# Kernel optimization log

Measured on AMD Instinct MI355X. Metric: run time of the kernel, lower is better.

Reference implementation:

```python
import jax, jax.numpy as jnp
import numpy as np

# Hyperparameters matching GyroLoss(__init__)
W = 1.0e6        # w
MIN_N = 4        # min_N -> min_train_freq = 16
MAX_N = 5        # max_N -> max_train_freq = 32
DT = 0.01        # dt (100 Hz IMU)
HUBER = 0.005    # huber delta
N0 = 5           # warm-up steps dropped from the residual
MIN_TRAIN_FREQ = 2 ** MIN_N


def _skew(v):
    # v: [M,3] -> [M,3,3] skew-symmetric matrices
    x, y, z = v[..., 0], v[..., 1], v[..., 2]
    o = jnp.zeros_like(x)
    return jnp.stack([
        jnp.stack([o, -z,  y], -1),
        jnp.stack([z,  o, -x], -1),
        jnp.stack([-y, x,  o], -1),
    ], -2)


def so3_exp(phi):
    # Rodrigues formula, phi: [M,3] -> R: [M,3,3]
    sq = jnp.sum(phi * phi, -1, keepdims=True)          # [M,1]
    angle = jnp.sqrt(jnp.maximum(sq, 1e-16))
    small = sq < 1e-12
    a = jnp.where(small, 1.0, angle)
    s = jnp.where(small, 1.0 - sq / 6.0, jnp.sin(a) / a)
    c = jnp.where(small, 0.5 - sq / 24.0, (1.0 - jnp.cos(a)) / (a * a))
    K = _skew(phi)
    I = jnp.eye(3, dtype=phi.dtype)
    return I + s[..., None] * K + c[..., None] * jnp.matmul(K, K)


def so3_log(R):
    # R: [M,3,3] -> phi: [M,3]
    tr = R[..., 0, 0] + R[..., 1, 1] + R[..., 2, 2]
    cos = jnp.clip(0.5 * (tr - 1.0), -1.0 + 1e-7, 1.0 - 1e-7)
    angle = jnp.arccos(cos)
    s = angle / (2.0 * jnp.sin(angle))
    vee = jnp.stack([
        R[..., 2, 1] - R[..., 1, 2],
        R[..., 0, 2] - R[..., 2, 0],
        R[..., 1, 0] - R[..., 0, 1],
    ], -1)
    return s[..., None] * vee


def _bmtm(a, b):
    # batched a^T @ b for [M,3,3]
    return jnp.einsum('nij,nik->njk', a, b)


def _f_huber(rs):
    # SmoothL1Loss (beta=1, mean reduction) on rs/HUBER vs zeros, scaled by w*huber^2
    z = rs / HUBER
    az = jnp.abs(z)
    l = jnp.mean(jnp.where(az < 1.0, 0.5 * z * z, az - 0.5))
    return W * l * HUBER ** 2


def setup_inputs() -> dict:
    key = jax.random.key(0)
    k1, k2, k3 = jax.random.split(key, 3)
    N, T = 64, 32768  # T divisible by 2**MAX_N
    xs = jax.random.normal(k1, (N, T, 3), dtype=jnp.float32)
    dp = jax.random.normal(k2, (1, 3), dtype=jnp.float32)  # unused by forward
    hat_xs = jax.random.normal(k3, (N, T, 3), dtype=jnp.float32)
    return {"xs": xs, "dp": dp, "hat_xs": hat_xs}


def reference(xs, dp, hat_xs):
    N = xs.shape[0]
    # ground-truth increments at min_train_freq stride -> rotations
    xs_r = so3_exp(xs[:, ::MIN_TRAIN_FREQ].reshape(-1, 3))       # [N*T/16,3,3]
    # predicted gyro -> per-step rotation increments
    Om = so3_exp((DT * hat_xs).reshape(-1, 3))                    # [N*T,3,3]
    # tree reduction: compose adjacent rotations min_N times
    for _ in range(MIN_N):
        Om = jnp.matmul(Om[::2], Om[1::2])
    rs = so3_log(_bmtm(Om, xs_r)).reshape(N, -1, 3)[:, N0:]
    loss = _f_huber(rs)
    for k in range(MIN_N, MAX_N):
        Om = jnp.matmul(Om[::2], Om[1::2])
        xs_r = jnp.matmul(xs_r[::2], xs_r[1::2])
        rs = so3_log(_bmtm(Om, xs_r)).reshape(N, -1, 3)[:, N0:]
        loss = loss + _f_huber(rs) / 2.0 ** (k - MIN_N + 1)
    return loss
```

## Files before the change

### kernel.cpp

```cpp
#include <hip/hip_runtime.h>
#include <math.h>

#define NSEQ 64
#define TLEN 32768
#define G16_PER_SEQ 2048
#define NG16 (NSEQ * G16_PER_SEQ)
#define N0 5
#define DT 0.01f
#define HUBER_INV 200.0f

__device__ __constant__ float C16 = 25.0f / (64.0f * 2043.0f * 3.0f);
__device__ __constant__ float C32 = 12.5f / (64.0f * 1019.0f * 3.0f);

__device__ __forceinline__ void mat_mul3(const float* A, const float* B, float* C) {
#pragma unroll
    for (int i = 0; i < 3; ++i) {
#pragma unroll
        for (int j = 0; j < 3; ++j) {
            C[3 * i + j] = A[3 * i + 0] * B[0 + j]
                         + A[3 * i + 1] * B[3 + j]
                         + A[3 * i + 2] * B[6 + j];
        }
    }
}

__device__ __forceinline__ void so3_exp_dev(float x, float y, float z, float* R) {
    float sq = x * x + y * y + z * z;
    float angle = sqrtf(fmaxf(sq, 1e-16f));
    bool small = sq < 1e-12f;
    float a = small ? 1.0f : angle;
    float sn, cs;
    __sincosf(a, &sn, &cs);
    float s = small ? (1.0f - sq * (1.0f / 6.0f)) : (sn / a);
    float c = small ? (0.5f - sq * (1.0f / 24.0f)) : ((1.0f - cs) / (a * a));
    float cxx = c * x * x, cyy = c * y * y, czz = c * z * z;
    float cxy = c * x * y, cxz = c * x * z, cyz = c * y * z;
    float sx = s * x, sy = s * y, sz = s * z;
    R[0] = 1.0f - cyy - czz; R[1] = cxy - sz;          R[2] = cxz + sy;
    R[3] = cxy + sz;         R[4] = 1.0f - cxx - czz;  R[5] = cyz - sx;
    R[6] = cxz - sy;         R[7] = cyz + sx;          R[8] = 1.0f - cxx - cyy;
}

__device__ __forceinline__ float huber3_bmtm_log(const float* Om, const float* Xr) {
    float M[9];
#pragma unroll
    for (int j = 0; j < 3; ++j) {
#pragma unroll
        for (int k = 0; k < 3; ++k) {
            M[3 * j + k] = Om[0 + j] * Xr[0 + k]
                         + Om[3 + j] * Xr[3 + k]
                         + Om[6 + j] * Xr[6 + k];
        }
    }
    float tr = M[0] + M[4] + M[8];
    float cosv = 0.5f * (tr - 1.0f);
    cosv = fminf(fmaxf(cosv, -1.0f + 1e-7f), 1.0f - 1e-7f);
    float angle = acosf(cosv);
    float sn = sqrtf(fmaxf(1.0f - cosv * cosv, 0.0f));
    float sfac = angle / (2.0f * sn);
    float v[3];
    v[0] = sfac * (M[7] - M[5]);
    v[1] = sfac * (M[2] - M[6]);
    v[2] = sfac * (M[3] - M[1]);
    float acc = 0.0f;
#pragma unroll
    for (int t = 0; t < 3; ++t) {
        float zz = v[t] * HUBER_INV;
        float az = fabsf(zz);
        acc += (az < 1.0f) ? 0.5f * zz * zz : az - 0.5f;
    }
    return acc;
}

__global__ void zero_out_kernel(float* out, int n) {
    int i = blockIdx.x * blockDim.x + threadIdx.x;
    if (i < n) out[i] = 0.0f;
}

__global__ __launch_bounds__(256) void gyro_loss_kernel(const float* __restrict__ xs,
                                                        const float* __restrict__ hat_xs,
                                                        float* __restrict__ out) {
    const int g = blockIdx.x * blockDim.x + threadIdx.x;

    const float4* hp = reinterpret_cast<const float4*>(hat_xs) + (size_t)g * 12;
    float hbuf[48];
#pragma unroll
    for (int q = 0; q < 12; ++q) {
        float4 vv = hp[q];
        hbuf[4 * q + 0] = vv.x; hbuf[4 * q + 1] = vv.y;
        hbuf[4 * q + 2] = vv.z; hbuf[4 * q + 3] = vv.w;
    }

    float Om[9];
    so3_exp_dev(DT * hbuf[0], DT * hbuf[1], DT * hbuf[2], Om);
#pragma unroll
    for (int i = 1; i < 16; ++i) {
        float Ri[9], tmp[9];
        so3_exp_dev(DT * hbuf[3 * i + 0], DT * hbuf[3 * i + 1], DT * hbuf[3 * i + 2], Ri);
        mat_mul3(Om, Ri, tmp);
#pragma unroll
        for (int t = 0; t < 9; ++t) Om[t] = tmp[t];
    }

    float4 xv = *(reinterpret_cast<const float4*>(xs) + (size_t)g * 12);
    float Xr[9];
    so3_exp_dev(xv.x, xv.y, xv.z, Xr);

    float partial = 0.0f;
    const int j = g & (G16_PER_SEQ - 1);
    if (j >= N0) partial += C16 * huber3_bmtm_log(Om, Xr);

    float OmN[9], XrN[9];
#pragma unroll
    for (int t = 0; t < 9; ++t) {
        OmN[t] = __shfl_down(Om[t], 1);
        XrN[t] = __shfl_down(Xr[t], 1);
    }
    if ((g & 1) == 0) {
        float Om32[9], Xr32[9];
        mat_mul3(Om, OmN, Om32);
        mat_mul3(Xr, XrN, Xr32);
        const int j2 = (g >> 1) & ((G16_PER_SEQ / 2) - 1);
        if (j2 >= N0) partial += C32 * huber3_bmtm_log(Om32, Xr32);
    }

#pragma unroll
    for (int off = 32; off > 0; off >>= 1) partial += __shfl_down(partial, off);

    __shared__ float wsum[4];
    const int lane = threadIdx.x & 63;
    const int wid = threadIdx.x >> 6;
    if (lane == 0) wsum[wid] = partial;
    __syncthreads();
    if (threadIdx.x == 0) {
        atomicAdd(out, wsum[0] + wsum[1] + wsum[2] + wsum[3]);
    }
}

extern "C" void kernel_launch(void* const* d_in, const int* in_sizes, int n_in,
                              void* d_out, int out_size, void* d_ws, size_t ws_size,
                              hipStream_t stream) {
    const float* xs     = (const float*)d_in[0];
    const float* hat_xs = (const float*)d_in[2];
    float* out = (float*)d_out;

    zero_out_kernel<<<1, 64, 0, stream>>>(out, out_size);
    gyro_loss_kernel<<<NG16 / 256, 256, 0, stream>>>(xs, hat_xs, out);
}
```

Baseline: 95.54 us.

## Split 16-step rotation chain across 4 lanes with shuffle tree and LDS staging

Each 16-step group is now handled by four threads that each compose four rotations, then combine them in order through xor-shuffle matrix products. The 32-step level reuses the same shuffle combine instead of a shift-down pair. hat_xs is staged through LDS with coalesced float4 loads. The global atomic is replaced by per-block partials summed in a second kernel. This gives four times more threads with shorter dependency chains and fewer registers per thread, at the cost of redundant xs loads and exp work on idle lanes plus an extra launch.

```diff
diff --git a/kernel.cpp b/kernel.cpp
--- a/kernel.cpp
+++ b/kernel.cpp
@@ -5,6 +5,10 @@
 #define TLEN 32768
 #define G16_PER_SEQ 2048
 #define NG16 (NSEQ * G16_PER_SEQ)
+#define STEPS_PER_THREAD 4
+#define NTHREADS (NG16 * 4)
+#define BLOCK 256
+#define NBLOCKS (NTHREADS / BLOCK)
 #define N0 5
 #define DT 0.01f
 #define HUBER_INV 200.0f
@@ -58,83 +62,95 @@
     float angle = acosf(cosv);
     float sn = sqrtf(fmaxf(1.0f - cosv * cosv, 0.0f));
     float sfac = angle / (2.0f * sn);
-    float v[3];
-    v[0] = sfac * (M[7] - M[5]);
-    v[1] = sfac * (M[2] - M[6]);
-    v[2] = sfac * (M[3] - M[1]);
+    float v0 = sfac * (M[7] - M[5]);
+    float v1 = sfac * (M[2] - M[6]);
+    float v2 = sfac * (M[3] - M[1]);
     float acc = 0.0f;
 #pragma unroll
     for (int t = 0; t < 3; ++t) {
-        float zz = v[t] * HUBER_INV;
+        float zz = (t == 0 ? v0 : (t == 1 ? v1 : v2)) * HUBER_INV;
         float az = fabsf(zz);
         acc += (az < 1.0f) ? 0.5f * zz * zz : az - 0.5f;
     }
     return acc;
 }
 
-__global__ void zero_out_kernel(float* out, int n) {
-    int i = blockIdx.x * blockDim.x + threadIdx.x;
-    if (i < n) out[i] = 0.0f;
+__device__ __forceinline__ void ordered_combine(float* A, int mask, bool upper) {
+    float L[9], R[9];
+#pragma unroll
+    for (int t = 0; t < 9; ++t) {
+        float b = __shfl_xor(A[t], mask);
+        L[t] = upper ? b : A[t];
+        R[t] = upper ? A[t] : b;
+    }
+    float C[9];
+    mat_mul3(L, R, C);
+#pragma unroll
+    for (int t = 0; t < 9; ++t) A[t] = C[t];
 }
 
-__global__ __launch_bounds__(256) void gyro_loss_kernel(const float* __restrict__ xs,
-                                                        const float* __restrict__ hat_xs,
-                                                        float* __restrict__ out) {
-    const int g = blockIdx.x * blockDim.x + threadIdx.x;
+__global__ __launch_bounds__(256, 4) void gyro_loss_kernel(const float* __restrict__ xs,
+                                                           const float* __restrict__ hat_xs,
+                                                           float* __restrict__ partials) {
+    __shared__ float lds[BLOCK * 12];
+    const int tid = threadIdx.x;
+    const int gt = blockIdx.x * BLOCK + tid;
 
-    const float4* hp = reinterpret_cast<const float4*>(hat_xs) + (size_t)g * 12;
-    float hbuf[48];
+    const float4* gp = reinterpret_cast<const float4*>(hat_xs) + (size_t)blockIdx.x * (BLOCK * 3);
+    float4* lp = reinterpret_cast<float4*>(lds);
 #pragma unroll
-    for (int q = 0; q < 12; ++q) {
-        float4 vv = hp[q];
-        hbuf[4 * q + 0] = vv.x; hbuf[4 * q + 1] = vv.y;
-        hbuf[4 * q + 2] = vv.z; hbuf[4 * q + 3] = vv.w;
-    }
+    for (int q = 0; q < 3; ++q) lp[q * BLOCK + tid] = gp[q * BLOCK + tid];
+    __syncthreads();
 
-    float Om[9];
-    so3_exp_dev(DT * hbuf[0], DT * hbuf[1], DT * hbuf[2], Om);
-#pragma unroll
-    for (int i = 1; i < 16; ++i) {
-        float Ri[9], tmp[9];
-        so3_exp_dev(DT * hbuf[3 * i + 0], DT * hbuf[3 * i + 1], DT * hbuf[3 * i + 2], Ri);
-        mat_mul3(Om, Ri, tmp);
-#pragma unroll
-        for (int t = 0; t < 9; ++t) Om[t] = tmp[t];
-    }
+    const float* h = &lds[12 * tid];
+    float Ra[9], Rb[9], P[9], Q[9], Om[9];
+    so3_exp_dev(DT * h[0], DT * h[1], DT * h[2], Ra);
+    so3_exp_dev(DT * h[3], DT * h[4], DT * h[5], Rb);
+    mat_mul3(Ra, Rb, P);
+    so3_exp_dev(DT * h[6], DT * h[7], DT * h[8], Ra);
+    so3_exp_dev(DT * h[9], DT * h[10], DT * h[11], Rb);
+    mat_mul3(Ra, Rb, Q);
+    mat_mul3(P, Q, Om);
+
+    ordered_combine(Om, 1, (tid & 1) != 0);
+    ordered_combine(Om, 2, (tid & 2) != 0);
+    const int g = gt >> 2;
 
     float4 xv = *(reinterpret_cast<const float4*>(xs) + (size_t)g * 12);
     float Xr[9];
     so3_exp_dev(xv.x, xv.y, xv.z, Xr);
 
     float partial = 0.0f;
-    const int j = g & (G16_PER_SEQ - 1);
-    if (j >= N0) partial += C16 * huber3_bmtm_log(Om, Xr);
+    if ((tid & 3) == 0 && (g & (G16_PER_SEQ - 1)) >= N0)
+        partial = C16 * huber3_bmtm_log(Om, Xr);
 
-    float OmN[9], XrN[9];
-#pragma unroll
-    for (int t = 0; t < 9; ++t) {
-        OmN[t] = __shfl_down(Om[t], 1);
-        XrN[t] = __shfl_down(Xr[t], 1);
-    }
-    if ((g & 1) == 0) {
-        float Om32[9], Xr32[9];
-        mat_mul3(Om, OmN, Om32);
-        mat_mul3(Xr, XrN, Xr32);
-        const int j2 = (g >> 1) & ((G16_PER_SEQ / 2) - 1);
-        if (j2 >= N0) partial += C32 * huber3_bmtm_log(Om32, Xr32);
-    }
+    ordered_combine(Om, 4, (tid & 4) != 0);
+    ordered_combine(Xr, 4, (tid & 4) != 0);
+    if ((tid & 7) == 0 && ((g >> 1) & (G16_PER_SEQ / 2 - 1)) >= N0)
+        partial += C32 * huber3_bmtm_log(Om, Xr);
 
 #pragma unroll
     for (int off = 32; off > 0; off >>= 1) partial += __shfl_down(partial, off);
-
     __shared__ float wsum[4];
-    const int lane = threadIdx.x & 63;
-    const int wid = threadIdx.x >> 6;
+    const int lane = tid & 63;
+    const int wid = tid >> 6;
     if (lane == 0) wsum[wid] = partial;
     __syncthreads();
-    if (threadIdx.x == 0) {
-        atomicAdd(out, wsum[0] + wsum[1] + wsum[2] + wsum[3]);
-    }
+    if (tid == 0) partials[blockIdx.x] = wsum[0] + wsum[1] + wsum[2] + wsum[3];
+}
+
+__global__ __launch_bounds__(256) void finish_kernel(const float* __restrict__ partials,
+                                                     float* __restrict__ out) {
+    const int tid = threadIdx.x;
+    float s = 0.0f;
+#pragma unroll
+    for (int q = 0; q < NBLOCKS / 256; ++q) s += partials[q * 256 + tid];
+#pragma unroll
+    for (int off = 32; off > 0; off >>= 1) s += __shfl_down(s, off);
+    __shared__ float wsum[4];
+    if ((tid & 63) == 0) wsum[tid >> 6] = s;
+    __syncthreads();
+    if (tid == 0) out[0] = wsum[0] + wsum[1] + wsum[2] + wsum[3];
 }
 
 extern "C" void kernel_launch(void* const* d_in, const int* in_sizes, int n_in,
@@ -143,7 +159,8 @@
     const float* xs     = (const float*)d_in[0];
     const float* hat_xs = (const float*)d_in[2];
     float* out = (float*)d_out;
+    float* partials = (float*)d_ws;
 
-    zero_out_kernel<<<1, 64, 0, stream>>>(out, out_size);
-    gyro_loss_kernel<<<NG16 / 256, 256, 0, stream>>>(xs, hat_xs, out);
+    gyro_loss_kernel<<<NBLOCKS, BLOCK, 0, stream>>>(xs, hat_xs, partials);
+    finish_kernel<<<1, 256, 0, stream>>>(partials, out);
 }
```

Result: no change. 96.43 us (+0.9%).
